# Performance work log

Hardware: AMD Instinct MI355X
Metric: run time of the kernel (lower is better)

## Reference

```python
import jax, jax.numpy as jnp
import numpy as np

TAU = 0.5  # threshold from init kwargs
INF = jnp.float32(1e30)


def setup_inputs() -> dict:
    key = jax.random.key(0)
    k1, k2 = jax.random.split(key)
    B, H, W = 16, 96, 96
    prediction = jax.random.uniform(k1, (B, H, W), dtype=jnp.float32)
    target = jax.random.uniform(k2, (B, H, W), dtype=jnp.float32)
    return {"prediction": prediction, "target": target}


def _grid_dist(H, W):
    # Euclidean distances between all (row, col) pixel coordinates -> [N, N]
    yy, xx = jnp.meshgrid(jnp.arange(H), jnp.arange(W), indexing="ij")
    coords = jnp.stack([yy.ravel(), xx.ravel()], axis=-1).astype(jnp.float32)  # [N, 2]
    sq = jnp.sum(coords * coords, axis=-1)  # [N]
    d2 = sq[:, None] + sq[None, :] - 2.0 * (coords @ coords.T)
    return jnp.sqrt(jnp.maximum(d2, 0.0))


def reference(prediction, target):
    B, H, W = prediction.shape
    N = H * W
    D = _grid_dist(H, W)  # shared across the batch: coord set is the full grid

    pred = (prediction >= TAU).reshape(B, N)   # bool masks selecting grid points
    label = (target >= TAU).reshape(B, N)

    def per_image(masks):
        a, b = masks  # bool [N], bool [N]
        any_a = jnp.any(a)
        any_b = jnp.any(b)
        # directed distances: for each point in one set, min dist to other set
        min_ab = jnp.min(jnp.where(b[None, :], D, INF), axis=1)   # [N]
        d_ab = jnp.max(jnp.where(a, min_ab, -INF))                # max over set A
        min_ba = jnp.min(jnp.where(a[:, None], D, INF), axis=0)   # [N]
        d_ba = jnp.max(jnp.where(b, min_ba, -INF))
        hd_both = jnp.maximum(d_ab, d_ba)
        # empty-set rules: one empty -> diameter of the other; both empty -> 0
        diam_a = jnp.max(jnp.where(a[:, None] & a[None, :], D, -INF))
        diam_b = jnp.max(jnp.where(b[:, None] & b[None, :], D, -INF))
        return jnp.where(
            any_a & any_b,
            hd_both,
            jnp.where(any_a, diam_a, jnp.where(any_b, diam_b, jnp.float32(0.0))),
        )

    # sequential over batch to keep peak memory at one [N, N] masked buffer
    hd = jax.lax.map(per_image, (pred, label))  # [B]
    return jnp.mean(hd)  # reduction == 'mean'
```

## Files before the change

kernel.cpp:

```cpp
#include <hip/hip_runtime.h>
#include <limits.h>

#define HB 16
#define HH 96
#define HW 96
#define HN (HH*HW)
#define WPR 3
#define WPI (HH*WPR)
#define STRIPES 12
#define ROWS_PER (HH/STRIPES)
#define PX_PER (ROWS_PER*HW)

__global__ __launch_bounds__(256) void mask_build(const float* __restrict__ pred,
                                                  const float* __restrict__ targ,
                                                  unsigned int* __restrict__ mA,
                                                  unsigned int* __restrict__ mB) {
    int i = blockIdx.x * 256 + threadIdx.x;
    float pv = pred[i], tv = targ[i];
    unsigned long long balA = __ballot(pv >= 0.5f);
    unsigned long long balB = __ballot(tv >= 0.5f);
    if ((threadIdx.x & 63) == 0) {
        int img = i / HN;
        int f = i - img * HN;
        int w = img * WPI + (f >> 5);
        mA[w]   = (unsigned int)balA;
        mA[w+1] = (unsigned int)(balA >> 32);
        mB[w]   = (unsigned int)balB;
        mB[w+1] = (unsigned int)(balB >> 32);
    }
}

__device__ __forceinline__ int nearest_dx(unsigned long long lo, unsigned int hi, int x) {
    int dr = 1 << 20, dl = 1 << 20;
    if (x < 64) {
        unsigned long long r = lo >> x;
        if (r) dr = __builtin_ctzll(r);
        else if (hi) dr = (64 - x) + __builtin_ctz(hi);
        unsigned long long lm = lo << (63 - x);
        if (lm) dl = __builtin_clzll(lm);
    } else {
        int xh = x - 64;
        unsigned int r = hi >> xh;
        if (r) dr = __builtin_ctz(r);
        unsigned int lmh = hi << (31 - xh);
        if (lmh) dl = __builtin_clz(lmh);
        else if (lo) dl = (xh + 1) + __builtin_clzll(lo);
    }
    return min(dl, dr);
}

__device__ __forceinline__ int search2d(const unsigned int* __restrict__ m, int y, int x) {
    int best = INT_MAX;
    for (int dy = 0; dy < HH; ++dy) {
        if (dy * dy >= best) break;
        int yl = y - dy;
        if (yl >= 0) {
            unsigned long long lo = (unsigned long long)m[yl*WPR] |
                                    ((unsigned long long)m[yl*WPR+1] << 32);
            unsigned int hi = m[yl*WPR+2];
            if (lo | hi) {
                int dx = nearest_dx(lo, hi, x);
                best = min(best, dy*dy + dx*dx);
            }
        }
        int yh = y + dy;
        if (dy > 0 && yh < HH) {
            unsigned long long lo = (unsigned long long)m[yh*WPR] |
                                    ((unsigned long long)m[yh*WPR+1] << 32);
            unsigned int hi = m[yh*WPR+2];
            if (lo | hi) {
                int dx = nearest_dx(lo, hi, x);
                best = min(best, dy*dy + dx*dx);
            }
        }
    }
    return best;
}

__global__ __launch_bounds__(256) void search_pass(const unsigned int* __restrict__ mA,
                                                   const unsigned int* __restrict__ mB,
                                                   int* __restrict__ maxAB2,
                                                   int* __restrict__ maxBA2) {
    int img    = blockIdx.x / STRIPES;
    int stripe = blockIdx.x - img * STRIPES;
    int tid = threadIdx.x;
    __shared__ unsigned int sA[WPI], sB[WPI];
    __shared__ int redAB, redBA;
    for (int w = tid; w < WPI; w += 256) {
        sA[w] = mA[img*WPI + w];
        sB[w] = mB[img*WPI + w];
    }
    if (tid == 0) { redAB = -1; redBA = -1; }
    __syncthreads();

    int lAB = -1, lBA = -1;
    #pragma unroll
    for (int k = 0; k < PX_PER; k += 256) {
        int li = k + tid;
        int ry = li / HW;
        int y  = stripe * ROWS_PER + ry;
        int x  = li - ry * HW;
        bool a = (sA[y*WPR + (x>>5)] >> (x & 31)) & 1u;
        bool b = (sB[y*WPR + (x>>5)] >> (x & 31)) & 1u;
        if (a) lAB = max(lAB, search2d(sB, y, x));
        if (b) lBA = max(lBA, search2d(sA, y, x));
    }
    atomicMax(&redAB, lAB);
    atomicMax(&redBA, lBA);
    __syncthreads();
    if (tid == 0) {
        atomicMax(&maxAB2[img], redAB);
        atomicMax(&maxBA2[img], redBA);
    }
}

__global__ void finalize(const float* __restrict__ pred,
                         const float* __restrict__ targ,
                         const int* __restrict__ maxAB2,
                         const int* __restrict__ maxBA2,
                         float* __restrict__ out) {
    __shared__ float hd[HB];
    __shared__ int diam2;
    int tid = threadIdx.x;

    if (tid < HB) {
        int mAB = maxAB2[tid], mBA = maxBA2[tid];
        bool anyA = mAB >= 0, anyB = mBA >= 0;
        float v;
        if (anyA && anyB)        v = sqrtf((float)max(mAB, mBA));
        else if (!anyA && !anyB) v = 0.0f;
        else                     v = -1.0f;
        hd[tid] = v;
    }
    __syncthreads();

    for (int img = 0; img < HB; ++img) {
        if (hd[img] >= 0.0f) continue;
        bool anyA = maxAB2[img] >= 0;
        const float* src = anyA ? pred : targ;
        if (tid == 0) diam2 = 0;
        __syncthreads();
        int local = 0;
        for (int i = tid; i < HN; i += blockDim.x) {
            if (src[img * HN + i] >= 0.5f) {
                int yi = i / HW, xi = i - (i / HW) * HW;
                for (int j = 0; j < HN; ++j) {
                    if (src[img * HN + j] >= 0.5f) {
                        int yj = j / HW, xj = j - (j / HW) * HW;
                        int dy = yi - yj, dx = xi - xj;
                        local = max(local, dy * dy + dx * dx);
                    }
                }
            }
        }
        atomicMax(&diam2, local);
        __syncthreads();
        if (tid == 0) hd[img] = sqrtf((float)diam2);
        __syncthreads();
    }

    if (tid == 0) {
        float sum = 0.0f;
        for (int i = 0; i < HB; ++i) sum += hd[i];
        out[0] = sum * (1.0f / HB);
    }
}

extern "C" void kernel_launch(void* const* d_in, const int* in_sizes, int n_in,
                              void* d_out, int out_size, void* d_ws, size_t ws_size,
                              hipStream_t stream) {
    const float* pred = (const float*)d_in[0];
    const float* targ = (const float*)d_in[1];
    float* out = (float*)d_out;

    unsigned int* mA = (unsigned int*)d_ws;
    unsigned int* mB = mA + HB * WPI;
    int* maxAB2 = (int*)(mB + HB * WPI);
    int* maxBA2 = maxAB2 + HB;

    hipMemsetAsync(maxAB2, 0xFF, 2 * HB * sizeof(int), stream);

    mask_build<<<HB * HN / 256, 256, 0, stream>>>(pred, targ, mA, mB);
    search_pass<<<HB * STRIPES, 256, 0, stream>>>(mA, mB, maxAB2, maxBA2);
    finalize<<<1, 256, 0, stream>>>(pred, targ, maxAB2, maxBA2, out);
}
```

Baseline: 71.50 us.

## Fuse mask build, Hausdorff search and finalize into one kernel per image

Replaces the three-kernel pipeline (mask build, striped search, single-block finalize) with one kernel that has one 1024-thread block per image. Each block builds its bitmasks in shared memory from float4 loads, runs the nearest-neighbour row search, reduces with wave shuffles and atomically adds its share of the mean. The empty-set diameter case now uses a bitmask farthest-point scan instead of the O(N^2) pixel loop. This removes launch overhead and the global mask round trip. In exchange only 16 blocks run, so parallelism across CUs is far lower than the previous 192 blocks.

```diff
diff --git a/kernel.cpp b/kernel.cpp
--- a/kernel.cpp
+++ b/kernel.cpp
@@ -7,28 +7,8 @@
 #define HN (HH*HW)
 #define WPR 3
 #define WPI (HH*WPR)
-#define STRIPES 12
-#define ROWS_PER (HH/STRIPES)
-#define PX_PER (ROWS_PER*HW)
-
-__global__ __launch_bounds__(256) void mask_build(const float* __restrict__ pred,
-                                                  const float* __restrict__ targ,
-                                                  unsigned int* __restrict__ mA,
-                                                  unsigned int* __restrict__ mB) {
-    int i = blockIdx.x * 256 + threadIdx.x;
-    float pv = pred[i], tv = targ[i];
-    unsigned long long balA = __ballot(pv >= 0.5f);
-    unsigned long long balB = __ballot(tv >= 0.5f);
-    if ((threadIdx.x & 63) == 0) {
-        int img = i / HN;
-        int f = i - img * HN;
-        int w = img * WPI + (f >> 5);
-        mA[w]   = (unsigned int)balA;
-        mA[w+1] = (unsigned int)(balA >> 32);
-        mB[w]   = (unsigned int)balB;
-        mB[w+1] = (unsigned int)(balB >> 32);
-    }
-}
+#define TPB 1024
+#define PXT (HN/TPB)
 
 __device__ __forceinline__ int nearest_dx(unsigned long long lo, unsigned int hi, int x) {
     int dr = 1 << 20, dl = 1 << 20;
@@ -49,7 +29,13 @@
     return min(dl, dr);
 }
 
-__device__ __forceinline__ int search2d(const unsigned int* __restrict__ m, int y, int x) {
+__device__ __forceinline__ int farthest_dx(unsigned long long lo, unsigned int hi, int x) {
+    int first = lo ? __builtin_ctzll(lo) : 64 + __builtin_ctz(hi);
+    int last  = hi ? 95 - __builtin_clz(hi) : 63 - __builtin_clzll(lo);
+    return max(x - first, last - x);
+}
+
+__device__ __forceinline__ int search2d(const unsigned int* m, int y, int x) {
     int best = INT_MAX;
     for (int dy = 0; dy < HH; ++dy) {
         if (dy * dy >= best) break;
@@ -77,92 +63,101 @@
     return best;
 }
 
-__global__ __launch_bounds__(256) void search_pass(const unsigned int* __restrict__ mA,
-                                                   const unsigned int* __restrict__ mB,
-                                                   int* __restrict__ maxAB2,
-                                                   int* __restrict__ maxBA2) {
-    int img    = blockIdx.x / STRIPES;
-    int stripe = blockIdx.x - img * STRIPES;
+__device__ __forceinline__ int farthest2d(const unsigned int* m, int y, int x) {
+    int best = 0;
+    for (int yy = 0; yy < HH; ++yy) {
+        unsigned long long lo = (unsigned long long)m[yy*WPR] |
+                                ((unsigned long long)m[yy*WPR+1] << 32);
+        unsigned int hi = m[yy*WPR+2];
+        if (lo | hi) {
+            int fd = farthest_dx(lo, hi, x);
+            int dy = yy - y;
+            best = max(best, dy*dy + fd*fd);
+        }
+    }
+    return best;
+}
+
+__global__ __launch_bounds__(TPB) void hausdorff_fused(const float* __restrict__ pred,
+                                                       const float* __restrict__ targ,
+                                                       float* __restrict__ out) {
+    int img = blockIdx.x;
     int tid = threadIdx.x;
     __shared__ unsigned int sA[WPI], sB[WPI];
     __shared__ int redAB, redBA;
-    for (int w = tid; w < WPI; w += 256) {
-        sA[w] = mA[img*WPI + w];
-        sB[w] = mB[img*WPI + w];
-    }
-    if (tid == 0) { redAB = -1; redBA = -1; }
-    __syncthreads();
+    __shared__ int fA, fB;
 
-    int lAB = -1, lBA = -1;
-    #pragma unroll
-    for (int k = 0; k < PX_PER; k += 256) {
-        int li = k + tid;
-        int ry = li / HW;
-        int y  = stripe * ROWS_PER + ry;
-        int x  = li - ry * HW;
-        bool a = (sA[y*WPR + (x>>5)] >> (x & 31)) & 1u;
-        bool b = (sB[y*WPR + (x>>5)] >> (x & 31)) & 1u;
-        if (a) lAB = max(lAB, search2d(sB, y, x));
-        if (b) lBA = max(lBA, search2d(sA, y, x));
-    }
-    atomicMax(&redAB, lAB);
-    atomicMax(&redBA, lBA);
-    __syncthreads();
-    if (tid == 0) {
-        atomicMax(&maxAB2[img], redAB);
-        atomicMax(&maxBA2[img], redBA);
-    }
-}
+    if (tid == 0) { redAB = -1; redBA = -1; fA = 0; fB = 0; }
 
-__global__ void finalize(const float* __restrict__ pred,
-                         const float* __restrict__ targ,
-                         const int* __restrict__ maxAB2,
-                         const int* __restrict__ maxBA2,
-                         float* __restrict__ out) {
-    __shared__ float hd[HB];
-    __shared__ int diam2;
-    int tid = threadIdx.x;
-
-    if (tid < HB) {
-        int mAB = maxAB2[tid], mBA = maxBA2[tid];
-        bool anyA = mAB >= 0, anyB = mBA >= 0;
-        float v;
-        if (anyA && anyB)        v = sqrtf((float)max(mAB, mBA));
-        else if (!anyA && !anyB) v = 0.0f;
-        else                     v = -1.0f;
-        hd[tid] = v;
+    if (tid < 2 * WPI) {
+        int set = tid >= WPI;
+        int w   = set ? tid - WPI : tid;
+        const float* src = (set ? targ : pred) + img * HN + 32 * w;
+        const float4* v4 = reinterpret_cast<const float4*>(src);
+        unsigned int bits = 0;
+        #pragma unroll
+        for (int j = 0; j < 8; ++j) {
+            float4 v = v4[j];
+            if (v.x >= 0.5f) bits |= 1u << (4*j + 0);
+            if (v.y >= 0.5f) bits |= 1u << (4*j + 1);
+            if (v.z >= 0.5f) bits |= 1u << (4*j + 2);
+            if (v.w >= 0.5f) bits |= 1u << (4*j + 3);
+        }
+        (set ? sB : sA)[w] = bits;
+        if (bits) { if (set) fB = 1; else fA = 1; }
     }
     __syncthreads();
 
-    for (int img = 0; img < HB; ++img) {
-        if (hd[img] >= 0.0f) continue;
-        bool anyA = maxAB2[img] >= 0;
-        const float* src = anyA ? pred : targ;
-        if (tid == 0) diam2 = 0;
-        __syncthreads();
-        int local = 0;
-        for (int i = tid; i < HN; i += blockDim.x) {
-            if (src[img * HN + i] >= 0.5f) {
-                int yi = i / HW, xi = i - (i / HW) * HW;
-                for (int j = 0; j < HN; ++j) {
-                    if (src[img * HN + j] >= 0.5f) {
-                        int yj = j / HW, xj = j - (j / HW) * HW;
-                        int dy = yi - yj, dx = xi - xj;
-                        local = max(local, dy * dy + dx * dx);
-                    }
-                }
-            }
+    bool anyA = fA != 0, anyB = fB != 0;
+    int lAB = -1, lBA = -1;
+
+    if (anyA && anyB) {
+        #pragma unroll
+        for (int k = 0; k < PXT; ++k) {
+            int li = k * TPB + tid;
+            int y  = li / HW;
+            int x  = li - y * HW;
+            bool a = (sA[y*WPR + (x>>5)] >> (x & 31)) & 1u;
+            bool b = (sB[y*WPR + (x>>5)] >> (x & 31)) & 1u;
+            if (a) lAB = max(lAB, search2d(sB, y, x));
+            if (b) lBA = max(lBA, search2d(sA, y, x));
         }
-        atomicMax(&diam2, local);
-        __syncthreads();
-        if (tid == 0) hd[img] = sqrtf((float)diam2);
-        __syncthreads();
+    } else if (anyA) {
+        for (int k = 0; k < PXT; ++k) {
+            int li = k * TPB + tid;
+            int y  = li / HW;
+            int x  = li - y * HW;
+            bool a = (sA[y*WPR + (x>>5)] >> (x & 31)) & 1u;
+            if (a) lAB = max(lAB, farthest2d(sA, y, x));
+        }
+    } else if (anyB) {
+        for (int k = 0; k < PXT; ++k) {
+            int li = k * TPB + tid;
+            int y  = li / HW;
+            int x  = li - y * HW;
+            bool b = (sB[y*WPR + (x>>5)] >> (x & 31)) & 1u;
+            if (b) lBA = max(lBA, farthest2d(sB, y, x));
+        }
     }
 
+    #pragma unroll
+    for (int off = 32; off >= 1; off >>= 1) {
+        lAB = max(lAB, __shfl_down(lAB, off, 64));
+        lBA = max(lBA, __shfl_down(lBA, off, 64));
+    }
+    if ((tid & 63) == 0) {
+        atomicMax(&redAB, lAB);
+        atomicMax(&redBA, lBA);
+    }
+    __syncthreads();
+
     if (tid == 0) {
-        float sum = 0.0f;
-        for (int i = 0; i < HB; ++i) sum += hd[i];
-        out[0] = sum * (1.0f / HB);
+        float hd;
+        if (anyA && anyB)      hd = sqrtf((float)max(redAB, redBA));
+        else if (anyA)         hd = sqrtf((float)redAB);
+        else if (anyB)         hd = sqrtf((float)redBA);
+        else                   hd = 0.0f;
+        atomicAdd(out, hd * (1.0f / HB));
     }
 }
 
@@ -173,14 +168,6 @@
     const float* targ = (const float*)d_in[1];
     float* out = (float*)d_out;
 
-    unsigned int* mA = (unsigned int*)d_ws;
-    unsigned int* mB = mA + HB * WPI;
-    int* maxAB2 = (int*)(mB + HB * WPI);
-    int* maxBA2 = maxAB2 + HB;
-
-    hipMemsetAsync(maxAB2, 0xFF, 2 * HB * sizeof(int), stream);
-
-    mask_build<<<HB * HN / 256, 256, 0, stream>>>(pred, targ, mA, mB);
-    search_pass<<<HB * STRIPES, 256, 0, stream>>>(mA, mB, maxAB2, maxBA2);
-    finalize<<<1, 256, 0, stream>>>(pred, targ, maxAB2, maxBA2, out);
+    hipMemsetAsync(out, 0, sizeof(float), stream);
+    hausdorff_fused<<<HB, TPB, 0, stream>>>(pred, targ, out);
 }
```

Result: slower. 76.85 us (+7.5%).
